# Kernel tuning notes

Measured on AMD Instinct MI355X. Metric: run time of the kernel, lower is better.

The kernel has to match this reference:

```python
import jax, jax.numpy as jnp
import numpy as np

E = 8       # num experts
D = 768     # embed_dim
H = 12      # num heads
F = 3072    # expert hidden = 4*D
TOPK = 2


def setup_inputs() -> dict:
    key = jax.random.key(0)
    ks = jax.random.split(key, 8)
    B, S = 4, 1024
    s = lambda d: 1.0 / np.sqrt(d)
    return {
        "x": jax.random.normal(ks[0], (B, S, D), jnp.float32),
        "w_qkv": jax.random.normal(ks[1], (D, 3 * D), jnp.float32) * s(D),
        "b_qkv": jnp.zeros((3 * D,), jnp.float32),
        "w_o": jax.random.normal(ks[2], (D, D), jnp.float32) * s(D),
        "b_o": jnp.zeros((D,), jnp.float32),
        "w_router": jax.random.normal(ks[3], (D, E), jnp.float32) * s(D),
        "w1": jax.random.normal(ks[4], (E, D, F), jnp.float32) * s(D),
        "b1": jnp.zeros((E, F), jnp.float32),
        "w2": jax.random.normal(ks[5], (E, F, D), jnp.float32) * s(F),
        "b2": jnp.zeros((E, D), jnp.float32),
    }


def reference(x, w_qkv, b_qkv, w_o, b_o, w_router, w1, b1, w2, b2):
    B, S, Dm = x.shape
    hd = Dm // H
    # --- multi-head self-attention ---
    qkv = x @ w_qkv + b_qkv                                  # [B,S,3D]
    q, k, v = jnp.split(qkv, 3, axis=-1)
    resh = lambda t: t.reshape(B, S, H, hd).transpose(0, 2, 1, 3)  # [B,H,S,hd]
    q, k, v = resh(q), resh(k), resh(v)
    scores = jnp.einsum('bhqd,bhkd->bhqk', q, k) / np.sqrt(hd).astype(np.float32)
    attn = jax.nn.softmax(scores, axis=-1)
    ctx = jnp.einsum('bhqk,bhkd->bhqd', attn, v)
    ctx = ctx.transpose(0, 2, 1, 3).reshape(B, S, Dm)
    y = ctx @ w_o + b_o                                      # [B,S,D]
    # --- top-k MoE feed-forward ---
    t = y.reshape(B * S, Dm)                                 # [T,D]
    logits = t @ w_router                                    # [T,E]
    probs = jax.nn.softmax(logits, axis=-1)
    topv, topi = jax.lax.top_k(probs, TOPK)                  # [T,K]
    topw = topv / jnp.sum(topv, axis=-1, keepdims=True)      # renormalized gates
    T = t.shape[0]
    wfull = jnp.zeros_like(probs).at[jnp.arange(T)[:, None], topi].set(topw)  # [T,E]
    # dense all-expert compute, weighted combine (faithful to routed math)
    h = jax.nn.gelu(jnp.einsum('td,edf->etf', t, w1) + b1[:, None, :])  # [E,T,F]
    oe = jnp.einsum('etf,efd->etd', h, w2) + b2[:, None, :]              # [E,T,D]
    out = jnp.einsum('te,etd->td', wfull, oe).reshape(B, S, Dm)
    diagnostics = probs  # router probabilities as diagnostics
    return (out, diagnostics)
```

## Files before the change

### kernel.cpp

```cpp
#include <hip/hip_runtime.h>
#include <hip/hip_bf16.h>
#include <cstdint>
#include <cmath>

#define T_TOK 4096
#define DIM   768
#define HEADS 12
#define HD    64
#define NEXP  8
#define FDIM  3072

typedef __attribute__((ext_vector_type(8))) short short8v;
typedef __attribute__((ext_vector_type(4))) float float4v;

__device__ __forceinline__ float gelu_tanh(float x) {
  float u = 0.7978845608028654f * (x + 0.044715f * x * x * x);
  return 0.5f * x * (1.0f + tanhf(u));
}

__device__ __forceinline__ short f2bf(float x) {
  __hip_bfloat16 h = __float2bfloat16(x);
  return *reinterpret_cast<short*>(&h);
}

__device__ __forceinline__ void gld16(void* lds, const void* g) {
  __builtin_amdgcn_global_load_lds(
      (__attribute__((address_space(1))) void*)(uintptr_t)g,
      (__attribute__((address_space(3))) void*)(uint32_t)(uintptr_t)lds,
      16, 0, 0);
}

template<int TBM, int TBN, bool BFOUT>
__global__ __launch_bounds__(256) void gemm_f32(
    const float* __restrict__ A, const float* __restrict__ W,
    const float* __restrict__ bias, float* __restrict__ C,
    short* __restrict__ Cbf, int M, int N, int K)
{
  constexpr int MM = TBM / 16;
  constexpr int MN = TBN / 16;
  constexpr int AL4 = TBM / 64;
  constexpr int BL4 = TBN / 64;
  __shared__ float As[16][TBM + 4];
  __shared__ float Bs[16][TBN + 4];
  const int bm = blockIdx.y * TBM;
  const int bn = blockIdx.x * TBN;
  const int tid = threadIdx.x;
  const int tr = tid >> 4;
  const int tc = tid & 15;

  float acc[MM][MN] = {};

  for (int k0 = 0; k0 < K; k0 += 16) {
    #pragma unroll
    for (int i = 0; i < AL4; i++) {
      int fidx = tid + i * 256;
      int row = fidx >> 2, c4 = fidx & 3;
      float4 v = *(const float4*)&A[(size_t)(bm + row) * K + k0 + c4 * 4];
      As[c4 * 4 + 0][row] = v.x;
      As[c4 * 4 + 1][row] = v.y;
      As[c4 * 4 + 2][row] = v.z;
      As[c4 * 4 + 3][row] = v.w;
    }
    #pragma unroll
    for (int i = 0; i < BL4; i++) {
      int fidx = tid + i * 256;
      int kk = fidx / (TBN / 4), n4 = fidx % (TBN / 4);
      *(float4*)&Bs[kk][n4 * 4] =
          *(const float4*)&W[(size_t)(k0 + kk) * N + bn + n4 * 4];
    }
    __syncthreads();
    #pragma unroll
    for (int kk = 0; kk < 16; kk++) {
      float a[MM], b[MN];
      #pragma unroll
      for (int u4 = 0; u4 < MM / 4; u4++) {
        float4 t = *(const float4*)&As[kk][tr * MM + u4 * 4];
        a[u4*4+0]=t.x; a[u4*4+1]=t.y; a[u4*4+2]=t.z; a[u4*4+3]=t.w;
      }
      #pragma unroll
      for (int v4 = 0; v4 < MN / 4; v4++) {
        float4 t = *(const float4*)&Bs[kk][tc * MN + v4 * 4];
        b[v4*4+0]=t.x; b[v4*4+1]=t.y; b[v4*4+2]=t.z; b[v4*4+3]=t.w;
      }
      #pragma unroll
      for (int u = 0; u < MM; u++)
        #pragma unroll
        for (int v = 0; v < MN; v++)
          acc[u][v] = fmaf(a[u], b[v], acc[u][v]);
    }
    __syncthreads();
  }

  #pragma unroll
  for (int u = 0; u < MM; u++) {
    int row = bm + tr * MM + u;
    #pragma unroll
    for (int v4 = 0; v4 < MN / 4; v4++) {
      int col = bn + tc * MN + v4 * 4;
      float4 o;
      o.x = acc[u][v4*4+0] + bias[col+0];
      o.y = acc[u][v4*4+1] + bias[col+1];
      o.z = acc[u][v4*4+2] + bias[col+2];
      o.w = acc[u][v4*4+3] + bias[col+3];
      *(float4*)&C[(size_t)row * N + col] = o;
      if (BFOUT) {
        short4 s = make_short4(f2bf(o.x), f2bf(o.y), f2bf(o.z), f2bf(o.w));
        *(short4*)&Cbf[(size_t)row * N + col] = s;
      }
    }
  }
}

__global__ __launch_bounds__(256) void transpose_bf16(
    const float* __restrict__ W, short* __restrict__ WT, int K, int N)
{
  __shared__ float t[32][33];
  const size_t mat = (size_t)K * N;
  const float* Wp = W + blockIdx.z * mat;
  short* WTp = WT + blockIdx.z * mat;
  int n0 = blockIdx.x * 32, k0 = blockIdx.y * 32;
  int tx = threadIdx.x, ty = threadIdx.y;
  #pragma unroll
  for (int i = 0; i < 4; i++)
    t[ty + i * 8][tx] = Wp[(size_t)(k0 + ty + i * 8) * N + n0 + tx];
  __syncthreads();
  #pragma unroll
  for (int i = 0; i < 4; i++)
    WTp[(size_t)(n0 + ty + i * 8) * K + k0 + tx] = f2bf(t[tx][ty + i * 8]);
}

template<int MODE>
__global__ __launch_bounds__(256) void moe_mm(
    const short* __restrict__ A, const short* __restrict__ WT,
    const float* __restrict__ bias, void* __restrict__ Cout,
    int N, int K,
    const int* __restrict__ offsets, const int* __restrict__ perm,
    const int* __restrict__ tmap, const int* __restrict__ tilecnt)
{
  const int bx = blockIdx.x;
  if (bx >= tilecnt[0]) return;
  const int info  = tmap[bx];
  const int e     = info >> 16;
  const int start = offsets[e];
  const int M     = offsets[e + 1] - start;
  const int bm    = (info & 0xffff) * 128;
  const int bn    = blockIdx.y * 128;

  __shared__ short As[4][128][8];
  __shared__ short Bs[4][128][8];
  __shared__ int   perm_s[128];

  const int tid  = threadIdx.x;
  const int lane = tid & 63;
  const int wave = tid >> 6;
  const int wm = wave >> 1, wn = wave & 1;
  const int lr = lane & 15;
  const int kb = lane >> 4;

  const short* WTe = WT + (size_t)e * ((size_t)N * K);
  const float* be  = bias + (size_t)e * N;

  if (MODE == 1) {
    if (tid < 128) {
      int rr = bm + tid;
      perm_s[tid] = (rr < M) ? perm[start + rr] : perm[start];
    }
    __syncthreads();
  }

  const short* asrc0;
  const short* asrc1;
  if (MODE == 1) {
    asrc0 = A + (size_t)perm_s[lane] * K + wave * 8;
    asrc1 = A + (size_t)perm_s[64 + lane] * K + wave * 8;
  } else {
    int r0 = bm + lane;      if (r0 >= M) r0 = M - 1;
    int r1 = bm + 64 + lane; if (r1 >= M) r1 = M - 1;
    asrc0 = A + (size_t)(start + r0) * K + wave * 8;
    asrc1 = A + (size_t)(start + r1) * K + wave * 8;
  }
  const short* bsrc0 = WTe + (size_t)(bn + lane) * K + wave * 8;
  const short* bsrc1 = WTe + (size_t)(bn + 64 + lane) * K + wave * 8;
  short* adst0 = &As[wave][0][0];
  short* adst1 = &As[wave][64][0];
  short* bdst0 = &Bs[wave][0][0];
  short* bdst1 = &Bs[wave][64][0];

  float4v acc[4][4] = {};

  for (int k0 = 0; k0 < K; k0 += 32) {
    __syncthreads();
    gld16(adst0, asrc0 + k0);
    gld16(adst1, asrc1 + k0);
    gld16(bdst0, bsrc0 + k0);
    gld16(bdst1, bsrc1 + k0);
    __syncthreads();

    short8v af[4], bfv[4];
    #pragma unroll
    for (int mi = 0; mi < 4; mi++)
      af[mi] = *(const short8v*)&As[kb][wm * 64 + mi * 16 + lr][0];
    #pragma unroll
    for (int ni = 0; ni < 4; ni++)
      bfv[ni] = *(const short8v*)&Bs[kb][wn * 64 + ni * 16 + lr][0];
    #pragma unroll
    for (int mi = 0; mi < 4; mi++)
      #pragma unroll
      for (int ni = 0; ni < 4; ni++)
        acc[mi][ni] = __builtin_amdgcn_mfma_f32_16x16x32_bf16(
            af[mi], bfv[ni], acc[mi][ni], 0, 0, 0);
  }

  #pragma unroll
  for (int ni = 0; ni < 4; ni++) {
    int col = bn + wn * 64 + ni * 16 + lr;
    float b = be[col];
    #pragma unroll
    for (int mi = 0; mi < 4; mi++) {
      int lrow0 = wm * 64 + mi * 16 + kb * 4;
      #pragma unroll
      for (int r = 0; r < 4; r++) {
        int rr = bm + lrow0 + r;
        if (rr < M) {
          if (MODE == 1) {
            short* C = (short*)Cout;
            C[(size_t)(start + rr) * N + col] = f2bf(gelu_tanh(acc[mi][ni][r] + b));
          } else {
            float* C = (float*)Cout;
            C[(size_t)(start + rr) * N + col] = acc[mi][ni][r] + b;
          }
        }
      }
    }
  }
}

__global__ __launch_bounds__(256) void combine_kernel(
    const float* __restrict__ oe, const int* __restrict__ ppos,
    const float* __restrict__ topg, float* __restrict__ out)
{
  int g = blockIdx.x * 256 + threadIdx.x;
  int t = g / 192;
  int c = (g - t * 192) * 4;
  int p0 = ppos[2 * t], p1 = ppos[2 * t + 1];
  float g0 = topg[2 * t], g1 = topg[2 * t + 1];
  float4 a = *(const float4*)&oe[(size_t)p0 * DIM + c];
  float4 b = *(const float4*)&oe[(size_t)p1 * DIM + c];
  float4 o;
  o.x = g0 * a.x + g1 * b.x;
  o.y = g0 * a.y + g1 * b.y;
  o.z = g0 * a.z + g1 * b.z;
  o.w = g0 * a.w + g1 * b.w;
  *(float4*)&out[(size_t)t * DIM + c] = o;
}

__global__ __launch_bounds__(512) void attn_kernel(
    const float* __restrict__ qkv, float* __restrict__ ctx)
{
  const int qt = blockIdx.x;
  const int bh = blockIdx.y;
  const int b = bh / HEADS, h = bh % HEADS;
  const float* base = qkv + (size_t)b * 1024 * (3 * DIM) + h * 64;

  __shared__ float ks[64 * 64];
  __shared__ float vs[64 * 64];
  __shared__ float lred[2][2][32];

  const int tid   = threadIdx.x;
  const int wv    = tid >> 6;
  const int qhalf = wv & 1;
  const int kq    = wv >> 1;
  const int lane  = tid & 63;
  const int grp   = lane >> 2;
  const int sub   = lane & 3;
  const int q0    = qhalf * 32 + grp * 2;
  const int dpart = sub * 16;

  const float qscale = 0.125f * 1.44269504088896f;
  float qA[16], qB[16], accA[16] = {}, accB[16] = {};
  float lA = 0.f, lB = 0.f;

  {
    const float* qpA = base + (size_t)(qt * 64 + q0) * (3 * DIM) + dpart;
    const float* qpB = qpA + 3 * DIM;
    #pragma unroll
    for (int d4 = 0; d4 < 4; d4++) {
      float4 ta = *(const float4*)(qpA + d4 * 4);
      float4 tb = *(const float4*)(qpB + d4 * 4);
      qA[d4*4+0]=ta.x*qscale; qA[d4*4+1]=ta.y*qscale; qA[d4*4+2]=ta.z*qscale; qA[d4*4+3]=ta.w*qscale;
      qB[d4*4+0]=tb.x*qscale; qB[d4*4+1]=tb.y*qscale; qB[d4*4+2]=tb.z*qscale; qB[d4*4+3]=tb.w*qscale;
    }
  }

  for (int kt = 0; kt < 16; kt++) {
    __syncthreads();
    #pragma unroll
    for (int i = 0; i < 2; i++) {
      int idx = tid + i * 512;
      int r = idx >> 4, c4 = idx & 15;
      const float* kp = base + (size_t)(kt * 64 + r) * (3 * DIM) + c4 * 4;
      *(float4*)&ks[r * 64 + c4 * 4] = *(const float4*)(kp + DIM);
      *(float4*)&vs[r * 64 + c4 * 4] = *(const float4*)(kp + 2 * DIM);
    }
    __syncthreads();

    #pragma unroll 2
    for (int jj = 0; jj < 16; jj++) {
      int j = kq * 16 + jj;
      float4 k0v = *(const float4*)&ks[j * 64 + dpart];
      float4 k1v = *(const float4*)&ks[j * 64 + dpart + 4];
      float4 k2v = *(const float4*)&ks[j * 64 + dpart + 8];
      float4 k3v = *(const float4*)&ks[j * 64 + dpart + 12];
      float a0, a1, a2, a3, b0, b1, b2, b3;
      a0  = qA[0]  * k0v.x; a0 = fmaf(qA[1],  k0v.y, a0);
      a0  = fmaf(qA[2],  k0v.z, a0); a0 = fmaf(qA[3],  k0v.w, a0);
      a1  = qA[4]  * k1v.x; a1 = fmaf(qA[5],  k1v.y, a1);
      a1  = fmaf(qA[6],  k1v.z, a1); a1 = fmaf(qA[7],  k1v.w, a1);
      a2  = qA[8]  * k2v.x; a2 = fmaf(qA[9],  k2v.y, a2);
      a2  = fmaf(qA[10], k2v.z, a2); a2 = fmaf(qA[11], k2v.w, a2);
      a3  = qA[12] * k3v.x; a3 = fmaf(qA[13], k3v.y, a3);
      a3  = fmaf(qA[14], k3v.z, a3); a3 = fmaf(qA[15], k3v.w, a3);
      b0  = qB[0]  * k0v.x; b0 = fmaf(qB[1],  k0v.y, b0);
      b0  = fmaf(qB[2],  k0v.z, b0); b0 = fmaf(qB[3],  k0v.w, b0);
      b1  = qB[4]  * k1v.x; b1 = fmaf(qB[5],  k1v.y, b1);
      b1  = fmaf(qB[6],  k1v.z, b1); b1 = fmaf(qB[7],  k1v.w, b1);
      b2  = qB[8]  * k2v.x; b2 = fmaf(qB[9],  k2v.y, b2);
      b2  = fmaf(qB[10], k2v.z, b2); b2 = fmaf(qB[11], k2v.w, b2);
      b3  = qB[12] * k3v.x; b3 = fmaf(qB[13], k3v.y, b3);
      b3  = fmaf(qB[14], k3v.z, b3); b3 = fmaf(qB[15], k3v.w, b3);
      float sA = (a0 + a1) + (a2 + a3);
      float sB = (b0 + b1) + (b2 + b3);
      sA += __shfl_xor(sA, 1);  sB += __shfl_xor(sB, 1);
      sA += __shfl_xor(sA, 2);  sB += __shfl_xor(sB, 2);
      float pA = exp2f(sA);
      float pB = exp2f(sB);
      lA += pA;  lB += pB;
      float4 v0v = *(const float4*)&vs[j * 64 + dpart];
      float4 v1v = *(const float4*)&vs[j * 64 + dpart + 4];
      float4 v2v = *(const float4*)&vs[j * 64 + dpart + 8];
      float4 v3v = *(const float4*)&vs[j * 64 + dpart + 12];
      float vr[16] = {v0v.x,v0v.y,v0v.z,v0v.w, v1v.x,v1v.y,v1v.z,v1v.w,
                      v2v.x,v2v.y,v2v.z,v2v.w, v3v.x,v3v.y,v3v.z,v3v.w};
      #pragma unroll
      for (int d = 0; d < 16; d++) {
        accA[d] = fmaf(pA, vr[d], accA[d]);
        accB[d] = fmaf(pB, vr[d], accB[d]);
      }
    }
  }

  float* regA = ks + qhalf * 2048;
  float* regB = vs + qhalf * 2048;
  const int r0 = (grp * 2) * 64 + dpart;
  const int r1 = r0 + 64;

  __syncthreads();
  if (kq == 2 || kq == 3) {
    float* buf = (kq == 2) ? regA : regB;
    #pragma unroll
    for (int d4 = 0; d4 < 4; d4++) {
      *(float4*)&buf[r0 + d4*4] =
          make_float4(accA[d4*4], accA[d4*4+1], accA[d4*4+2], accA[d4*4+3]);
      *(float4*)&buf[r1 + d4*4] =
          make_float4(accB[d4*4], accB[d4*4+1], accB[d4*4+2], accB[d4*4+3]);
    }
    if (sub == 0) {
      lred[kq - 2][qhalf][grp * 2]     = lA;
      lred[kq - 2][qhalf][grp * 2 + 1] = lB;
    }
  }
  __syncthreads();
  if (kq == 0 || kq == 1) {
    const float* buf = (kq == 0) ? regA : regB;
    #pragma unroll
    for (int d4 = 0; d4 < 4; d4++) {
      float4 a = *(const float4*)&buf[r0 + d4*4];
      float4 c = *(const float4*)&buf[r1 + d4*4];
      accA[d4*4+0] += a.x; accA[d4*4+1] += a.y; accA[d4*4+2] += a.z; accA[d4*4+3] += a.w;
      accB[d4*4+0] += c.x; accB[d4*4+1] += c.y; accB[d4*4+2] += c.z; accB[d4*4+3] += c.w;
    }
    lA += lred[kq][qhalf][grp * 2];
    lB += lred[kq][qhalf][grp * 2 + 1];
  }
  __syncthreads();
  if (kq == 1) {
    #pragma unroll
    for (int d4 = 0; d4 < 4; d4++) {
      *(float4*)&regA[r0 + d4*4] =
          make_float4(accA[d4*4], accA[d4*4+1], accA[d4*4+2], accA[d4*4+3]);
      *(float4*)&regA[r1 + d4*4] =
          make_float4(accB[d4*4], accB[d4*4+1], accB[d4*4+2], accB[d4*4+3]);
    }
    if (sub == 0) {
      lred[0][qhalf][grp * 2]     = lA;
      lred[0][qhalf][grp * 2 + 1] = lB;
    }
  }
  __syncthreads();
  if (kq == 0) {
    #pragma unroll
    for (int d4 = 0; d4 < 4; d4++) {
      float4 a = *(const float4*)&regA[r0 + d4*4];
      float4 c = *(const float4*)&regA[r1 + d4*4];
      accA[d4*4+0] += a.x; accA[d4*4+1] += a.y; accA[d4*4+2] += a.z; accA[d4*4+3] += a.w;
      accB[d4*4+0] += c.x; accB[d4*4+1] += c.y; accB[d4*4+2] += c.z; accB[d4*4+3] += c.w;
    }
    lA += lred[0][qhalf][grp * 2];
    lB += lred[0][qhalf][grp * 2 + 1];
    float invA = 1.f / lA, invB = 1.f / lB;
    float* opA = ctx + ((size_t)b * 1024 + qt * 64 + q0) * DIM + h * 64 + dpart;
    float* opB = opA + DIM;
    #pragma unroll
    for (int d4 = 0; d4 < 4; d4++) {
      float4 oa, ob;
      oa.x = accA[d4*4+0]*invA; oa.y = accA[d4*4+1]*invA;
      oa.z = accA[d4*4+2]*invA; oa.w = accA[d4*4+3]*invA;
      ob.x = accB[d4*4+0]*invB; ob.y = accB[d4*4+1]*invB;
      ob.z = accB[d4*4+2]*invB; ob.w = accB[d4*4+3]*invB;
      *(float4*)(opA + d4 * 4) = oa;
      *(float4*)(opB + d4 * 4) = ob;
    }
  }
}

__global__ __launch_bounds__(256) void router_kernel(
    const float* __restrict__ y, const float* __restrict__ wr,
    float* __restrict__ probs, int* __restrict__ topi,
    float* __restrict__ topg, int* __restrict__ counts)
{
  __shared__ float w[DIM * NEXP];
  const int tid = threadIdx.x;
  for (int i = tid; i < DIM * NEXP; i += 256) w[i] = wr[i];
  __syncthreads();

  const int t = blockIdx.x * 256 + tid;
  const float* yp = y + (size_t)t * DIM;
  float logit[8] = {};
  for (int d = 0; d < DIM; d++) {
    float xv = yp[d];
    #pragma unroll
    for (int e = 0; e < 8; e++) logit[e] = fmaf(xv, w[d * 8 + e], logit[e]);
  }
  float mx = logit[0];
  #pragma unroll
  for (int e = 1; e < 8; e++) mx = fmaxf(mx, logit[e]);
  float p[8], sum = 0.f;
  #pragma unroll
  for (int e = 0; e < 8; e++) { p[e] = __expf(logit[e] - mx); sum += p[e]; }
  float inv = 1.f / sum;
  #pragma unroll
  for (int e = 0; e < 8; e++) { p[e] *= inv; probs[(size_t)t * 8 + e] = p[e]; }

  int i0 = 0;
  #pragma unroll
  for (int e = 1; e < 8; e++) if (p[e] > p[i0]) i0 = e;
  int i1 = (i0 == 0) ? 1 : 0;
  #pragma unroll
  for (int e = 0; e < 8; e++) if (e != i0 && p[e] > p[i1]) i1 = e;
  float g = p[i0] + p[i1];
  topi[2 * t] = i0;  topi[2 * t + 1] = i1;
  topg[2 * t] = p[i0] / g;  topg[2 * t + 1] = p[i1] / g;
  atomicAdd(&counts[i0], 1);
  atomicAdd(&counts[i1], 1);
}

__global__ void init_meta(int* counts) {
  if (threadIdx.x < 8) counts[threadIdx.x] = 0;
}

__global__ void scan_kernel(const int* __restrict__ counts,
                            int* __restrict__ offsets, int* __restrict__ cursors,
                            int* __restrict__ tmap, int* __restrict__ tilecnt) {
  if (threadIdx.x == 0) {
    int s = 0;
    for (int e = 0; e < 8; e++) { offsets[e] = s; cursors[e] = s; s += counts[e]; }
    offsets[8] = s;
    int tu = 0;
    for (int e = 0; e < 8; e++) {
      int m = counts[e];
      for (int t = 0; t * 128 < m; t++) tmap[tu++] = (e << 16) | t;
    }
    tilecnt[0] = tu;
  }
}

__global__ __launch_bounds__(256) void scatter_kernel(
    const int* __restrict__ topi, int* __restrict__ cursors,
    int* __restrict__ perm, int* __restrict__ ppos)
{
  const int t = blockIdx.x * 256 + threadIdx.x;
  #pragma unroll
  for (int s = 0; s < 2; s++) {
    int e = topi[2 * t + s];
    int pos = atomicAdd(&cursors[e], 1);
    perm[pos] = t;
    ppos[2 * t + s] = pos;
  }
}

extern "C" void kernel_launch(void* const* d_in, const int* in_sizes, int n_in,
                              void* d_out, int out_size, void* d_ws, size_t ws_size,
                              hipStream_t stream) {
  const float* x        = (const float*)d_in[0];
  const float* w_qkv    = (const float*)d_in[1];
  const float* b_qkv    = (const float*)d_in[2];
  const float* w_o      = (const float*)d_in[3];
  const float* b_o      = (const float*)d_in[4];
  const float* w_router = (const float*)d_in[5];
  const float* w1       = (const float*)d_in[6];
  const float* b1       = (const float*)d_in[7];
  const float* w2       = (const float*)d_in[8];
  const float* b2       = (const float*)d_in[9];

  float* out   = (float*)d_out;
  float* probs = out + (size_t)T_TOK * DIM;

  char* ws = (char*)d_ws;
  float* qkv  = (float*)ws;
  short* hbuf = (short*)ws;
  short* wT   = (short*)(ws + 50331648);
  float* ctx  = (float*)(ws + 88080384);
  float* oe   = (float*)(ws + 88080384);
  float* y    = (float*)(ws + 100663296);
  short* ybf  = (short*)(ws + 113246208);
  char*  meta = ws + 119537664;
  int*   counts  = (int*)meta;
  int*   cursors = counts + 8;
  int*   offsets = cursors + 8;
  int*   topi    = offsets + 16;
  float* topg    = (float*)(topi + 8192);
  int*   perm    = (int*)(topg + 8192);
  int*   ppos    = perm + 8192;
  int*   tmap    = ppos + 8192;
  int*   tilecnt = tmap + 80;

  init_meta<<<1, 64, 0, stream>>>(counts);

  gemm_f32<128, 64, false><<<dim3((3 * DIM) / 64, T_TOK / 128), 256, 0, stream>>>(
      x, w_qkv, b_qkv, qkv, nullptr, T_TOK, 3 * DIM, DIM);

  attn_kernel<<<dim3(16, 48), 512, 0, stream>>>(qkv, ctx);

  gemm_f32<64, 64, true><<<dim3(DIM / 64, T_TOK / 64), 256, 0, stream>>>(
      ctx, w_o, b_o, y, ybf, T_TOK, DIM, DIM);

  router_kernel<<<16, 256, 0, stream>>>(y, w_router, probs, topi, topg, counts);
  scan_kernel<<<1, 64, 0, stream>>>(counts, offsets, cursors, tmap, tilecnt);
  scatter_kernel<<<16, 256, 0, stream>>>(topi, cursors, perm, ppos);

  transpose_bf16<<<dim3(FDIM / 32, DIM / 32, NEXP), dim3(32, 8), 0, stream>>>(
      w1, wT, DIM, FDIM);
  moe_mm<1><<<dim3(72, FDIM / 128), 256, 0, stream>>>(
      ybf, wT, b1, hbuf, FDIM, DIM, offsets, perm, tmap, tilecnt);

  transpose_bf16<<<dim3(DIM / 32, FDIM / 32, NEXP), dim3(32, 8), 0, stream>>>(
      w2, wT, FDIM, DIM);
  moe_mm<2><<<dim3(72, DIM / 128), 256, 0, stream>>>(
      hbuf, wT, b2, oe, DIM, FDIM, offsets, perm, tmap, tilecnt);

  combine_kernel<<<(T_TOK * DIM / 4) / 256, 256, 0, stream>>>(oe, ppos, topg, out);
}
```

Baseline: 1.005 ms.

## Deepen MoE GEMM k-step, simplify attention dot product, widen QKV tile

The MoE bf16 GEMM now loads two 32-wide k-slices per barrier pair, using double-size LDS buffers, to halve the number of synchronizations per K. The attention QK dot product is rewritten as a single serial FMA chain instead of four partial sums. The QKV projection GEMM switches to a 128x128 tile. Together these aim to cut barrier overhead and improve reuse, at the cost of more shared memory and a longer dependent FMA chain in attention.

```diff
diff --git a/kernel.cpp b/kernel.cpp
--- a/kernel.cpp
+++ b/kernel.cpp
@@ -146,8 +146,8 @@
   const int bm    = (info & 0xffff) * 128;
   const int bn    = blockIdx.y * 128;
 
-  __shared__ short As[4][128][8];
-  __shared__ short Bs[4][128][8];
+  __shared__ short As[8][128][8];
+  __shared__ short Bs[8][128][8];
   __shared__ int   perm_s[128];
 
   const int tid  = threadIdx.x;
@@ -181,34 +181,37 @@
   }
   const short* bsrc0 = WTe + (size_t)(bn + lane) * K + wave * 8;
   const short* bsrc1 = WTe + (size_t)(bn + 64 + lane) * K + wave * 8;
-  short* adst0 = &As[wave][0][0];
-  short* adst1 = &As[wave][64][0];
-  short* bdst0 = &Bs[wave][0][0];
-  short* bdst1 = &Bs[wave][64][0];
 
   float4v acc[4][4] = {};
 
-  for (int k0 = 0; k0 < K; k0 += 32) {
-    __syncthreads();
-    gld16(adst0, asrc0 + k0);
-    gld16(adst1, asrc1 + k0);
-    gld16(bdst0, bsrc0 + k0);
-    gld16(bdst1, bsrc1 + k0);
-    __syncthreads();
-
-    short8v af[4], bfv[4];
-    #pragma unroll
-    for (int mi = 0; mi < 4; mi++)
-      af[mi] = *(const short8v*)&As[kb][wm * 64 + mi * 16 + lr][0];
-    #pragma unroll
-    for (int ni = 0; ni < 4; ni++)
-      bfv[ni] = *(const short8v*)&Bs[kb][wn * 64 + ni * 16 + lr][0];
-    #pragma unroll
-    for (int mi = 0; mi < 4; mi++)
+  for (int k0 = 0; k0 < K; k0 += 64) {
+    __syncthreads();
+    gld16(&As[wave][0][0],  asrc0 + k0);
+    gld16(&As[wave][64][0], asrc1 + k0);
+    gld16(&Bs[wave][0][0],  bsrc0 + k0);
+    gld16(&Bs[wave][64][0], bsrc1 + k0);
+    gld16(&As[wave + 4][0][0],  asrc0 + k0 + 32);
+    gld16(&As[wave + 4][64][0], asrc1 + k0 + 32);
+    gld16(&Bs[wave + 4][0][0],  bsrc0 + k0 + 32);
+    gld16(&Bs[wave + 4][64][0], bsrc1 + k0 + 32);
+    __syncthreads();
+
+    #pragma unroll
+    for (int hh = 0; hh < 2; hh++) {
+      short8v af[4], bfv[4];
+      #pragma unroll
+      for (int mi = 0; mi < 4; mi++)
+        af[mi] = *(const short8v*)&As[hh * 4 + kb][wm * 64 + mi * 16 + lr][0];
       #pragma unroll
       for (int ni = 0; ni < 4; ni++)
-        acc[mi][ni] = __builtin_amdgcn_mfma_f32_16x16x32_bf16(
-            af[mi], bfv[ni], acc[mi][ni], 0, 0, 0);
+        bfv[ni] = *(const short8v*)&Bs[hh * 4 + kb][wn * 64 + ni * 16 + lr][0];
+      #pragma unroll
+      for (int mi = 0; mi < 4; mi++)
+        #pragma unroll
+        for (int ni = 0; ni < 4; ni++)
+          acc[mi][ni] = __builtin_amdgcn_mfma_f32_16x16x32_bf16(
+              af[mi], bfv[ni], acc[mi][ni], 0, 0, 0);
+    }
   }
 
   #pragma unroll
@@ -311,25 +314,14 @@
       float4 k1v = *(const float4*)&ks[j * 64 + dpart + 4];
       float4 k2v = *(const float4*)&ks[j * 64 + dpart + 8];
       float4 k3v = *(const float4*)&ks[j * 64 + dpart + 12];
-      float a0, a1, a2, a3, b0, b1, b2, b3;
-      a0  = qA[0]  * k0v.x; a0 = fmaf(qA[1],  k0v.y, a0);
-      a0  = fmaf(qA[2],  k0v.z, a0); a0 = fmaf(qA[3],  k0v.w, a0);
-      a1  = qA[4]  * k1v.x; a1 = fmaf(qA[5],  k1v.y, a1);
-      a1  = fmaf(qA[6],  k1v.z, a1); a1 = fmaf(qA[7],  k1v.w, a1);
-      a2  = qA[8]  * k2v.x; a2 = fmaf(qA[9],  k2v.y, a2);
-      a2  = fmaf(qA[10], k2v.z, a2); a2 = fmaf(qA[11], k2v.w, a2);
-      a3  = qA[12] * k3v.x; a3 = fmaf(qA[13], k3v.y, a3);
-      a3  = fmaf(qA[14], k3v.z, a3); a3 = fmaf(qA[15], k3v.w, a3);
-      b0  = qB[0]  * k0v.x; b0 = fmaf(qB[1],  k0v.y, b0);
-      b0  = fmaf(qB[2],  k0v.z, b0); b0 = fmaf(qB[3],  k0v.w, b0);
-      b1  = qB[4]  * k1v.x; b1 = fmaf(qB[5],  k1v.y, b1);
-      b1  = fmaf(qB[6],  k1v.z, b1); b1 = fmaf(qB[7],  k1v.w, b1);
-      b2  = qB[8]  * k2v.x; b2 = fmaf(qB[9],  k2v.y, b2);
-      b2  = fmaf(qB[10], k2v.z, b2); b2 = fmaf(qB[11], k2v.w, b2);
-      b3  = qB[12] * k3v.x; b3 = fmaf(qB[13], k3v.y, b3);
-      b3  = fmaf(qB[14], k3v.z, b3); b3 = fmaf(qB[15], k3v.w, b3);
-      float sA = (a0 + a1) + (a2 + a3);
-      float sB = (b0 + b1) + (b2 + b3);
+      float kr[16] = {k0v.x,k0v.y,k0v.z,k0v.w, k1v.x,k1v.y,k1v.z,k1v.w,
+                      k2v.x,k2v.y,k2v.z,k2v.w, k3v.x,k3v.y,k3v.z,k3v.w};
+      float sA = 0.f, sB = 0.f;
+      #pragma unroll
+      for (int d = 0; d < 16; d++) {
+        sA = fmaf(qA[d], kr[d], sA);
+        sB = fmaf(qB[d], kr[d], sB);
+      }
       sA += __shfl_xor(sA, 1);  sB += __shfl_xor(sB, 1);
       sA += __shfl_xor(sA, 2);  sB += __shfl_xor(sB, 2);
       float pA = exp2f(sA);
@@ -536,7 +528,7 @@
 
   init_meta<<<1, 64, 0, stream>>>(counts);
 
-  gemm_f32<128, 64, false><<<dim3((3 * DIM) / 64, T_TOK / 128), 256, 0, stream>>>(
+  gemm_f32<128, 128, false><<<dim3((3 * DIM) / 128, T_TOK / 128), 256, 0, stream>>>(
       x, w_qkv, b_qkv, qkv, nullptr, T_TOK, 3 * DIM, DIM);
 
   attn_kernel<<<dim3(16, 48), 512, 0, stream>>>(qkv, ctx);
```

New measurement: 976.2 us. 2.9% less time.
